# Kernel tuning notes

Measured on AMD Instinct MI355X. Metric: run time of the kernel, lower is better.

## Reference

```python
import jax, jax.numpy as jnp
import numpy as np

B, NIN, H1, H2, NOUT, COND, FC = 64, 512, 1024, 1024, 512, 64, 1


def _made_masks():
    rng = np.random.RandomState(0)
    d_in = np.arange(1, NIN + 1)
    d1 = rng.randint(1, NIN, size=H1)
    d2 = rng.randint(1, NIN, size=H2)
    d_out = np.arange(1, NOUT + 1)
    m0 = (d1[:, None] >= d_in[None, :]).astype(np.float32)   # (H1, NIN)
    m1 = (d2[:, None] >= d1[None, :]).astype(np.float32)     # (H2, H1)
    m2 = (d_out[:, None] > d2[None, :]).astype(np.float32)   # (NOUT, H2)
    return m0, m1, m2


def setup_inputs() -> dict:
    key = jax.random.key(0)
    ks = jax.random.split(key, 20)
    m0, m1, m2 = _made_masks()

    def lin(k, o, i):  # fan-in scaled weight
        return jax.random.normal(k, (o, i), jnp.float32) / np.float32(np.sqrt(i))

    def vec(k, n):
        return jax.random.normal(k, (n,), jnp.float32) * 0.01

    return {
        "x": jax.random.normal(ks[0], (B, NIN), jnp.float32),
        "u": jax.random.normal(ks[1], (B, COND), jnp.float32),
        "mask0": jnp.asarray(m0), "mask1": jnp.asarray(m1), "mask2": jnp.asarray(m2),
        "W0": lin(ks[2], H1, NIN), "W1": lin(ks[3], H2, H1), "W2": lin(ks[4], NOUT, H2),
        "a0_w": lin(ks[5], FC * NIN, COND), "a0_b": vec(ks[6], FC * NIN),
        "b0_w": lin(ks[7], FC * H1, COND), "b0_b": vec(ks[8], FC * H1),
        "a1_w": lin(ks[9], FC * H1, COND), "a1_b": vec(ks[10], FC * H1),
        "b1_w": lin(ks[11], FC * H2, COND), "b1_b": vec(ks[12], FC * H2),
        "a2_w": lin(ks[13], FC * H2, COND), "a2_b": vec(ks[14], FC * H2),
        "b2_w": lin(ks[15], FC * NOUT, COND), "b2_b": vec(ks[16], FC * NOUT),
    }


def _cml(x, u, W, m, aw, ab, bw, bb):
    # ConditionedMaskedLinear.forward
    Bb = x.shape[0]
    o, i = W.shape
    f1 = (u @ aw.T + ab).reshape(Bb, FC, i)      # (B, F, in)
    f2 = (u @ bw.T + bb).reshape(Bb, o, FC)      # (B, out, F)
    cond_mask = jax.nn.sigmoid(jnp.einsum('bfi,bof->boi', f1, f2)) * (m * W)
    return jnp.einsum('boi,bi->bo', cond_mask, x)


def reference(x, u, mask0, mask1, mask2, W0, W1, W2,
              a0_w, a0_b, b0_w, b0_b,
              a1_w, a1_b, b1_w, b1_b,
              a2_w, a2_b, b2_w, b2_b):
    # ConditionalStrNN.forward applies ONLY the ConditionedMaskedLinear layers
    # (activations/norms in net_list are skipped by the isinstance check).
    h = _cml(x, u, W0, mask0, a0_w, a0_b, b0_w, b0_b)
    h = _cml(h, u, W1, mask1, a1_w, a1_b, b1_w, b1_b)
    h = _cml(h, u, W2, mask2, a2_w, a2_b, b2_w, b2_b)
    return h
```

## Files before the change

### kernel.cpp

```cpp
#include <hip/hip_runtime.h>

#define BB    64
#define NIN   512
#define H1D   1024
#define H2D   1024
#define NOUTD 512
#define CONDD 64
#define L2E   1.4426950408889634f

__global__ __launch_bounds__(256) void prep_kernel(
    const float* __restrict__ x,  const float* __restrict__ u,
    const float* __restrict__ a0w, const float* __restrict__ a0b,
    const float* __restrict__ b0w, const float* __restrict__ b0b,
    const float* __restrict__ a1w, const float* __restrict__ a1b,
    const float* __restrict__ b1w, const float* __restrict__ b1b,
    const float* __restrict__ a2w, const float* __restrict__ a2b,
    const float* __restrict__ b2w, const float* __restrict__ b2b,
    const float* __restrict__ m0, const float* __restrict__ m1,
    const float* __restrict__ m2,
    float* __restrict__ AX0, float* __restrict__ AX1, float* __restrict__ AX2,
    float* __restrict__ C0t, float* __restrict__ C1t, float* __restrict__ C2t,
    int* __restrict__ len1, int* __restrict__ len2, int* __restrict__ len3,
    int* __restrict__ key2)
{
    __shared__ float lds[64 * 65];
    const int tid = threadIdx.x;
    const int bid = blockIdx.x;

    if (bid < 320) {
        for (int e = tid; e < BB * CONDD; e += 256)
            lds[(e & 63) * 65 + (e >> 6)] = u[e];
        __syncthreads();

        const int b   = tid & 63;
        const int wid = __builtin_amdgcn_readfirstlane(tid >> 6);
        const int r0  = bid * 16 + wid * 4;

        const float* w; const float* bias; float* o; int stride; float scale; int lr0;
        if      (r0 <  512) { w = a0w; bias = a0b; o = AX0; stride = 2; scale = L2E; lr0 = r0;        }
        else if (r0 < 1536) { w = b0w; bias = b0b; o = C0t; stride = 1; scale = 1.f; lr0 = r0 -  512; }
        else if (r0 < 2560) { w = a1w; bias = a1b; o = AX1; stride = 2; scale = L2E; lr0 = r0 - 1536; }
        else if (r0 < 3584) { w = b1w; bias = b1b; o = C1t; stride = 1; scale = 1.f; lr0 = r0 - 2560; }
        else if (r0 < 4608) { w = a2w; bias = a2b; o = AX2; stride = 2; scale = L2E; lr0 = r0 - 3584; }
        else                { w = b2w; bias = b2b; o = C2t; stride = 1; scale = 1.f; lr0 = r0 - 4608; }

        const float* __restrict__ w0 = w + (lr0 + 0) * CONDD;
        const float* __restrict__ w1 = w + (lr0 + 1) * CONDD;
        const float* __restrict__ w2 = w + (lr0 + 2) * CONDD;
        const float* __restrict__ w3 = w + (lr0 + 3) * CONDD;
        float acc0 = bias[lr0 + 0], acc1 = bias[lr0 + 1];
        float acc2 = bias[lr0 + 2], acc3 = bias[lr0 + 3];
        #pragma unroll
        for (int k = 0; k < CONDD; ++k) {
            const float uv = lds[k * 65 + b];
            acc0 = fmaf(w0[k], uv, acc0);
            acc1 = fmaf(w1[k], uv, acc1);
            acc2 = fmaf(w2[k], uv, acc2);
            acc3 = fmaf(w3[k], uv, acc3);
        }
        o[((lr0 + 0) * 64 + b) * stride] = acc0 * scale;
        o[((lr0 + 1) * 64 + b) * stride] = acc1 * scale;
        o[((lr0 + 2) * 64 + b) * stride] = acc2 * scale;
        o[((lr0 + 3) * 64 + b) * stride] = acc3 * scale;
    } else if (bid < 328) {
        const int i0 = (bid - 320) * 64;
        for (int e = tid; e < 64 * 64; e += 256) {
            int r = e >> 6, c = e & 63;
            lds[c * 65 + r] = x[r * NIN + i0 + c];
        }
        __syncthreads();
        for (int e = tid; e < 64 * 64; e += 256) {
            int r = e >> 6, c = e & 63;
            AX0[((i0 + r) * 64 + c) * 2 + 1] = lds[r * 65 + c];
        }
    } else if (bid < 392) {
        const int l = tid & 63, w = tid >> 6;
        const int rb = (bid - 328) * 16 + w * 4;
        for (int j = 0; j < 4; ++j) {
            const int r = rb + j;
            const float4* rp = (const float4*)(m0 + (size_t)r * 512);
            const float4 A = rp[l], B = rp[l + 64];
            float s = A.x + A.y + A.z + A.w + B.x + B.y + B.z + B.w;
            #pragma unroll
            for (int d = 32; d; d >>= 1) s += __shfl_down(s, d);
            if (l == 0) len1[r] = (int)(s + 0.5f);
        }
    } else if (bid < 456) {
        const int l = tid & 63, w = tid >> 6;
        const int rb = (bid - 392) * 16 + w * 4;
        for (int j = 0; j < 4; ++j) {
            const int r = rb + j;
            const float4* rp = (const float4*)(m1 + (size_t)r * 1024);
            const float4 A = rp[l], B = rp[l + 64], C = rp[l + 128], D = rp[l + 192];
            float s = A.x + A.y + A.z + A.w + B.x + B.y + B.z + B.w
                    + C.x + C.y + C.z + C.w + D.x + D.y + D.z + D.w;
            #pragma unroll
            for (int d = 32; d; d >>= 1) s += __shfl_down(s, d);
            if (l == 0) len2[r] = (int)(s + 0.5f);
        }
    } else if (bid < 488) {
        const int l = tid & 63, w = tid >> 6;
        const int rb = (bid - 456) * 16 + w * 4;
        for (int j = 0; j < 4; ++j) {
            const int r = rb + j;
            const float4* rp = (const float4*)(m2 + (size_t)r * 1024);
            const float4 A = rp[l], B = rp[l + 64], C = rp[l + 128], D = rp[l + 192];
            float s = A.x + A.y + A.z + A.w + B.x + B.y + B.z + B.w
                    + C.x + C.y + C.z + C.w + D.x + D.y + D.z + D.w;
            #pragma unroll
            for (int d = 32; d; d >>= 1) s += __shfl_down(s, d);
            if (l == 0) len3[r] = (int)(s + 0.5f);
        }
    } else {
        const int cb  = bid - 488;
        const int c   = cb * 64 + (tid & 63);
        const int seg = tid >> 6;
        float s = 0.f;
        for (int j = 0; j < 128; ++j)
            s += m2[(size_t)(seg * 128 + j) * 1024 + c];
        lds[seg * 64 + (tid & 63)] = s;
        __syncthreads();
        if (tid < 64) {
            const float t = lds[tid] + lds[64 + tid] + lds[128 + tid] + lds[192 + tid];
            key2[cb * 64 + tid] = 512 - (int)(t + 0.5f);
        }
    }
}

__global__ __launch_bounds__(1024) void sort_kernel(
    const int* __restrict__ len1, const int* __restrict__ key2,
    const int* __restrict__ len2,
    int* __restrict__ order1, int* __restrict__ len1s,
    int* __restrict__ order2, int* __restrict__ len2s)
{
    __shared__ int hist[1024];
    __shared__ int scan[1024];
    const int t = threadIdx.x;
    const int* key = blockIdx.x ? key2 : len1;
    const int k = key[t];
    hist[t] = 0;
    __syncthreads();
    atomicAdd(&hist[k], 1);
    __syncthreads();
    scan[t] = hist[t];
    __syncthreads();
    for (int s = 1; s < 1024; s <<= 1) {
        const int v = scan[t] + ((t >= s) ? scan[t - s] : 0);
        __syncthreads();
        scan[t] = v;
        __syncthreads();
    }
    const int excl = scan[t] - hist[t];
    __syncthreads();
    hist[t] = excl;
    __syncthreads();
    const int pos = atomicAdd(&hist[k], 1);
    if (blockIdx.x == 0) {
        order1[pos] = t;
        len1s[pos]  = k;
    } else {
        order2[pos] = t;
        len2s[pos]  = len2[t];
    }
}

template<int I, int O, bool PR, bool GI, bool FINAL>
__global__ __launch_bounds__(1024) void gated(
    const float2* __restrict__ AX, const float* __restrict__ Ct,
    const float* __restrict__ W,  const int* __restrict__ lenS,
    const int* __restrict__ ordRow, const int* __restrict__ ordIn,
    float* __restrict__ out)
{
    constexpr int NB = O / 2;
    const int bid = blockIdx.x;
    const int k   = (bid < NB / 2) ? bid : (NB + NB / 2 - 1 - bid);
    const int R0  = 2 * k;
    const int tid = threadIdx.x;
    const int b   = tid & 63;
    const int wid = __builtin_amdgcn_readfirstlane(tid >> 6);

    __shared__ float2 mw[I];
    __shared__ int    ord[GI ? I : 1];
    __shared__ float  red[16][2][64];

    const int len0 = lenS[R0], len1 = lenS[R0 + 1];
    const int r0 = PR ? ordRow[R0]     : R0;
    const int r1 = PR ? ordRow[R0 + 1] : (R0 + 1);
    const int Lb  = (len0 > len1) ? len0 : len1;
    const int T   = (Lb + 15) >> 4;
    const int T16 = T << 4;

    const float* __restrict__ w0p = W + (size_t)r0 * I;
    const float* __restrict__ w1p = W + (size_t)r1 * I;
    for (int p = tid; p < T16; p += 1024) {
        const int ix = GI ? ordIn[p] : p;
        if (GI) ord[p] = ix;
        float2 v;
        v.x = (p < len0) ? w0p[ix] : 0.f;
        v.y = (p < len1) ? w1p[ix] : 0.f;
        mw[p] = v;
    }
    const float cc0 = Ct[r0 * 64 + b];
    const float cc1 = Ct[r1 * 64 + b];
    __syncthreads();

    float a0 = 0.f, a1 = 0.f;
    #pragma unroll 4
    for (int t = 0; t < T; ++t) {
        const int p  = wid + (t << 4);
        const int ix = GI ? ord[p] : p;
        const float2 ax = AX[(size_t)ix * 64 + b];
        const float2 w  = mw[p];
        const float e0 = __builtin_amdgcn_exp2f(-(ax.x * cc0));
        const float s0 = __builtin_amdgcn_rcpf(1.f + e0);
        const float e1 = __builtin_amdgcn_exp2f(-(ax.x * cc1));
        const float s1 = __builtin_amdgcn_rcpf(1.f + e1);
        a0 = fmaf(s0, w.x * ax.y, a0);
        a1 = fmaf(s1, w.y * ax.y, a1);
    }

    red[wid][0][b] = a0;
    red[wid][1][b] = a1;
    __syncthreads();
    if (tid < 128) {
        const int oo = tid >> 6, bb = tid & 63;
        float v = 0.f;
        #pragma unroll
        for (int q = 0; q < 16; ++q) v += red[q][oo][bb];
        const int r = oo ? r1 : r0;
        if (FINAL) out[bb * NOUTD + r] = v;
        else       out[((size_t)r * 64 + bb) * 2 + 1] = v;
    }
}

extern "C" void kernel_launch(void* const* d_in, const int* in_sizes, int n_in,
                              void* d_out, int out_size, void* d_ws, size_t ws_size,
                              hipStream_t stream) {
    (void)in_sizes; (void)n_in; (void)out_size; (void)ws_size;
    const float* x   = (const float*)d_in[0];
    const float* u   = (const float*)d_in[1];
    const float* m0  = (const float*)d_in[2];
    const float* m1  = (const float*)d_in[3];
    const float* m2  = (const float*)d_in[4];
    const float* W0  = (const float*)d_in[5];
    const float* W1  = (const float*)d_in[6];
    const float* W2  = (const float*)d_in[7];
    const float* a0w = (const float*)d_in[8];  const float* a0b = (const float*)d_in[9];
    const float* b0w = (const float*)d_in[10]; const float* b0b = (const float*)d_in[11];
    const float* a1w = (const float*)d_in[12]; const float* a1b = (const float*)d_in[13];
    const float* b1w = (const float*)d_in[14]; const float* b1b = (const float*)d_in[15];
    const float* a2w = (const float*)d_in[16]; const float* a2b = (const float*)d_in[17];
    const float* b2w = (const float*)d_in[18]; const float* b2b = (const float*)d_in[19];

    float* ws  = (float*)d_ws;
    float* AX0 = ws;
    float* AX1 = ws + 65536;
    float* AX2 = ws + 196608;
    float* C0t = ws + 327680;
    float* C1t = ws + 393216;
    float* C2t = ws + 458752;
    int*   ib  = (int*)(ws + 491520);
    int* len1   = ib;
    int* len2   = ib + 1024;
    int* len3   = ib + 2048;
    int* key2   = ib + 2560;
    int* order1 = ib + 3584;
    int* len1s  = ib + 4608;
    int* order2 = ib + 5632;
    int* len2s  = ib + 6656;
    float* out = (float*)d_out;

    prep_kernel<<<504, 256, 0, stream>>>(x, u,
        a0w, a0b, b0w, b0b, a1w, a1b, b1w, b1b, a2w, a2b, b2w, b2b,
        m0, m1, m2,
        AX0, AX1, AX2, C0t, C1t, C2t,
        len1, len2, len3, key2);

    sort_kernel<<<2, 1024, 0, stream>>>(len1, key2, len2,
                                        order1, len1s, order2, len2s);

    gated<NIN, H1D, true,  false, false><<<H1D / 2, 1024, 0, stream>>>(
        (const float2*)AX0, C0t, W0, len1s, order1, nullptr, AX1);
    gated<H1D, H2D, true,  true,  false><<<H2D / 2, 1024, 0, stream>>>(
        (const float2*)AX1, C1t, W1, len2s, order2, order1, AX2);
    gated<H2D, NOUTD, false, true, true><<<NOUTD / 2, 1024, 0, stream>>>(
        (const float2*)AX2, C2t, W2, len3, nullptr, order2, out);
}
```

Before: 144.1 us.

## Store next-layer activations in sorted order to remove gathers and use contiguous per-wave chunks

Each middle layer now writes its (A, x) pairs indexed by sorted row position, pairing its output with the next layer's precomputed A term. The next layer can then read AX contiguously without the ordIn gather from LDS. Each wave handles a contiguous chunk of the reduction with float4 weight loads and more independent accumulators, and the final layer becomes a 512-thread, one-row-per-block kernel. Zeroed padding regions, written by an extra sort-kernel block, let the chunked loops read past the valid length safely. The cost is extra workspace and a more complex indexing scheme.

After: 140.7 us. 1.02x faster.

```diff
diff --git a/kernel.cpp b/kernel.cpp
--- a/kernel.cpp
+++ b/kernel.cpp
@@ -18,7 +18,7 @@
     const float* __restrict__ b2w, const float* __restrict__ b2b,
     const float* __restrict__ m0, const float* __restrict__ m1,
     const float* __restrict__ m2,
-    float* __restrict__ AX0, float* __restrict__ AX1, float* __restrict__ AX2,
+    float* __restrict__ AX0, float* __restrict__ A1x, float* __restrict__ A2x,
     float* __restrict__ C0t, float* __restrict__ C1t, float* __restrict__ C2t,
     int* __restrict__ len1, int* __restrict__ len2, int* __restrict__ len3,
     int* __restrict__ key2)
@@ -39,9 +39,9 @@
         const float* w; const float* bias; float* o; int stride; float scale; int lr0;
         if      (r0 <  512) { w = a0w; bias = a0b; o = AX0; stride = 2; scale = L2E; lr0 = r0;        }
         else if (r0 < 1536) { w = b0w; bias = b0b; o = C0t; stride = 1; scale = 1.f; lr0 = r0 -  512; }
-        else if (r0 < 2560) { w = a1w; bias = a1b; o = AX1; stride = 2; scale = L2E; lr0 = r0 - 1536; }
+        else if (r0 < 2560) { w = a1w; bias = a1b; o = A1x; stride = 1; scale = L2E; lr0 = r0 - 1536; }
         else if (r0 < 3584) { w = b1w; bias = b1b; o = C1t; stride = 1; scale = 1.f; lr0 = r0 - 2560; }
-        else if (r0 < 4608) { w = a2w; bias = a2b; o = AX2; stride = 2; scale = L2E; lr0 = r0 - 3584; }
+        else if (r0 < 4608) { w = a2w; bias = a2b; o = A2x; stride = 1; scale = L2E; lr0 = r0 - 3584; }
         else                { w = b2w; bias = b2b; o = C2t; stride = 1; scale = 1.f; lr0 = r0 - 4608; }
 
         const float* __restrict__ w0 = w + (lr0 + 0) * CONDD;
@@ -131,8 +131,21 @@
     const int* __restrict__ len1, const int* __restrict__ key2,
     const int* __restrict__ len2,
     int* __restrict__ order1, int* __restrict__ len1s,
-    int* __restrict__ order2, int* __restrict__ len2s)
+    int* __restrict__ order2, int* __restrict__ len2s,
+    float4* __restrict__ pad0, float4* __restrict__ pad1,
+    float4* __restrict__ pad2)
 {
+    if (blockIdx.x == 2) {
+        const float4 z = {0.f, 0.f, 0.f, 0.f};
+        const int t = threadIdx.x;
+        #pragma unroll
+        for (int j = 0; j < 2; ++j) {
+            pad0[j * 1024 + t] = z;
+            pad1[j * 1024 + t] = z;
+            pad2[j * 1024 + t] = z;
+        }
+        return;
+    }
     __shared__ int hist[1024];
     __shared__ int scan[1024];
     const int t = threadIdx.x;
@@ -164,63 +177,64 @@
     }
 }
 
-template<int I, int O, bool PR, bool GI, bool FINAL>
-__global__ __launch_bounds__(1024) void gated(
+template<int I, bool GI>
+__global__ __launch_bounds__(1024) void gated_mid(
     const float2* __restrict__ AX, const float* __restrict__ Ct,
-    const float* __restrict__ W,  const int* __restrict__ lenS,
-    const int* __restrict__ ordRow, const int* __restrict__ ordIn,
-    float* __restrict__ out)
+    const float* __restrict__ W,  const float* __restrict__ Anext,
+    const int* __restrict__ lenS, const int* __restrict__ ordRow,
+    const int* __restrict__ ordIn, float2* __restrict__ outAX)
 {
-    constexpr int NB = O / 2;
     const int bid = blockIdx.x;
-    const int k   = (bid < NB / 2) ? bid : (NB + NB / 2 - 1 - bid);
+    const int k   = (bid < 256) ? bid : (767 - bid);
     const int R0  = 2 * k;
     const int tid = threadIdx.x;
     const int b   = tid & 63;
     const int wid = __builtin_amdgcn_readfirstlane(tid >> 6);
 
-    __shared__ float2 mw[I];
-    __shared__ int    ord[GI ? I : 1];
+    __shared__ float2 mw2[I + 64];
     __shared__ float  red[16][2][64];
 
     const int len0 = lenS[R0], len1 = lenS[R0 + 1];
-    const int r0 = PR ? ordRow[R0]     : R0;
-    const int r1 = PR ? ordRow[R0 + 1] : (R0 + 1);
-    const int Lb  = (len0 > len1) ? len0 : len1;
-    const int T   = (Lb + 15) >> 4;
-    const int T16 = T << 4;
+    const int r0 = ordRow[R0], r1 = ordRow[R0 + 1];
+    const int Lmax = (len0 > len1) ? len0 : len1;
+    const int Q = ((((Lmax + 1) >> 1) + 15) >> 4);
+    const int S = Q << 5;
 
     const float* __restrict__ w0p = W + (size_t)r0 * I;
     const float* __restrict__ w1p = W + (size_t)r1 * I;
-    for (int p = tid; p < T16; p += 1024) {
-        const int ix = GI ? ordIn[p] : p;
-        if (GI) ord[p] = ix;
+    for (int p = tid; p < S; p += 1024) {
+        const int ix = GI ? ((p < Lmax) ? ordIn[p] : 0) : p;
         float2 v;
         v.x = (p < len0) ? w0p[ix] : 0.f;
         v.y = (p < len1) ? w1p[ix] : 0.f;
-        mw[p] = v;
+        mw2[p] = v;
     }
     const float cc0 = Ct[r0 * 64 + b];
     const float cc1 = Ct[r1 * 64 + b];
     __syncthreads();
 
-    float a0 = 0.f, a1 = 0.f;
+    const int base = (wid * Q) << 1;
+    const float2* __restrict__ axp = AX + (size_t)base * 64 + b;
+    const float2* __restrict__ mwp = mw2 + base;
+
+    float a00 = 0.f, a01 = 0.f, a10 = 0.f, a11 = 0.f;
     #pragma unroll 4
-    for (int t = 0; t < T; ++t) {
-        const int p  = wid + (t << 4);
-        const int ix = GI ? ord[p] : p;
-        const float2 ax = AX[(size_t)ix * 64 + b];
-        const float2 w  = mw[p];
-        const float e0 = __builtin_amdgcn_exp2f(-(ax.x * cc0));
-        const float s0 = __builtin_amdgcn_rcpf(1.f + e0);
-        const float e1 = __builtin_amdgcn_exp2f(-(ax.x * cc1));
-        const float s1 = __builtin_amdgcn_rcpf(1.f + e1);
-        a0 = fmaf(s0, w.x * ax.y, a0);
-        a1 = fmaf(s1, w.y * ax.y, a1);
-    }
-
-    red[wid][0][b] = a0;
-    red[wid][1][b] = a1;
+    for (int t = 0; t < Q; ++t) {
+        const float4 m4  = *(const float4*)(mwp + 2 * t);
+        const float2 axa = axp[(size_t)(2 * t) * 64];
+        const float2 axb = axp[(size_t)(2 * t + 1) * 64];
+        const float e0 = __builtin_amdgcn_exp2f(-(axa.x * cc0));
+        const float e1 = __builtin_amdgcn_exp2f(-(axa.x * cc1));
+        const float e2 = __builtin_amdgcn_exp2f(-(axb.x * cc0));
+        const float e3 = __builtin_amdgcn_exp2f(-(axb.x * cc1));
+        a00 = fmaf(__builtin_amdgcn_rcpf(1.f + e0), m4.x * axa.y, a00);
+        a01 = fmaf(__builtin_amdgcn_rcpf(1.f + e1), m4.y * axa.y, a01);
+        a10 = fmaf(__builtin_amdgcn_rcpf(1.f + e2), m4.z * axb.y, a10);
+        a11 = fmaf(__builtin_amdgcn_rcpf(1.f + e3), m4.w * axb.y, a11);
+    }
+
+    red[wid][0][b] = a00 + a10;
+    red[wid][1][b] = a01 + a11;
     __syncthreads();
     if (tid < 128) {
         const int oo = tid >> 6, bb = tid & 63;
@@ -228,8 +242,66 @@
         #pragma unroll
         for (int q = 0; q < 16; ++q) v += red[q][oo][bb];
         const int r = oo ? r1 : r0;
-        if (FINAL) out[bb * NOUTD + r] = v;
-        else       out[((size_t)r * 64 + bb) * 2 + 1] = v;
+        float2 o2;
+        o2.x = Anext[r * 64 + bb];
+        o2.y = v;
+        outAX[(size_t)(R0 + oo) * 64 + bb] = o2;
+    }
+}
+
+__global__ __launch_bounds__(512) void gated_fin(
+    const float2* __restrict__ AX, const float* __restrict__ Ct,
+    const float* __restrict__ W,  const int* __restrict__ len3,
+    const int* __restrict__ ordIn, float* __restrict__ out)
+{
+    const int bid = blockIdx.x;
+    const int r   = (bid < 256) ? bid : (767 - bid);
+    const int tid = threadIdx.x;
+    const int b   = tid & 63;
+    const int wid = __builtin_amdgcn_readfirstlane(tid >> 6);
+
+    __shared__ float mw1[H2D + 64];
+    __shared__ float red[8][64];
+
+    const int len = len3[r];
+    const int Q   = (((len + 3) >> 2) + 7) >> 3;
+    const int S   = Q << 5;
+
+    const float* __restrict__ wp = W + (size_t)r * H2D;
+    for (int p = tid; p < S; p += 512)
+        mw1[p] = (p < len) ? wp[ordIn[p]] : 0.f;
+    const float cc = Ct[r * 64 + b];
+    __syncthreads();
+
+    const int base = (wid * Q) << 2;
+    const float2* __restrict__ axp = AX + (size_t)base * 64 + b;
+    const float*  __restrict__ mwp = mw1 + base;
+
+    float a0 = 0.f, a1 = 0.f, a2 = 0.f, a3 = 0.f;
+    #pragma unroll 4
+    for (int t = 0; t < Q; ++t) {
+        const float4 mm  = *(const float4*)(mwp + 4 * t);
+        const float2 x0 = axp[(size_t)(4 * t + 0) * 64];
+        const float2 x1 = axp[(size_t)(4 * t + 1) * 64];
+        const float2 x2 = axp[(size_t)(4 * t + 2) * 64];
+        const float2 x3 = axp[(size_t)(4 * t + 3) * 64];
+        const float e0 = __builtin_amdgcn_exp2f(-(x0.x * cc));
+        const float e1 = __builtin_amdgcn_exp2f(-(x1.x * cc));
+        const float e2 = __builtin_amdgcn_exp2f(-(x2.x * cc));
+        const float e3 = __builtin_amdgcn_exp2f(-(x3.x * cc));
+        a0 = fmaf(__builtin_amdgcn_rcpf(1.f + e0), mm.x * x0.y, a0);
+        a1 = fmaf(__builtin_amdgcn_rcpf(1.f + e1), mm.y * x1.y, a1);
+        a2 = fmaf(__builtin_amdgcn_rcpf(1.f + e2), mm.z * x2.y, a2);
+        a3 = fmaf(__builtin_amdgcn_rcpf(1.f + e3), mm.w * x3.y, a3);
+    }
+
+    red[wid][b] = (a0 + a1) + (a2 + a3);
+    __syncthreads();
+    if (tid < 64) {
+        float v = 0.f;
+        #pragma unroll
+        for (int q = 0; q < 8; ++q) v += red[q][tid];
+        out[tid * NOUTD + r] = v;
     }
 }
 
@@ -252,14 +324,16 @@
     const float* a2w = (const float*)d_in[16]; const float* a2b = (const float*)d_in[17];
     const float* b2w = (const float*)d_in[18]; const float* b2b = (const float*)d_in[19];
 
-    float* ws  = (float*)d_ws;
-    float* AX0 = ws;
-    float* AX1 = ws + 65536;
-    float* AX2 = ws + 196608;
-    float* C0t = ws + 327680;
-    float* C1t = ws + 393216;
-    float* C2t = ws + 458752;
-    int*   ib  = (int*)(ws + 491520);
+    float* ws   = (float*)d_ws;
+    float* AX0  = ws;
+    float* AX1s = ws + 73728;
+    float* AX2s = ws + 212992;
+    float* A1x  = ws + 352256;
+    float* A2x  = ws + 417792;
+    float* C0t  = ws + 483328;
+    float* C1t  = ws + 548864;
+    float* C2t  = ws + 614400;
+    int*   ib   = (int*)(ws + 647168);
     int* len1   = ib;
     int* len2   = ib + 1024;
     int* len3   = ib + 2048;
@@ -268,21 +342,28 @@
     int* len1s  = ib + 4608;
     int* order2 = ib + 5632;
     int* len2s  = ib + 6656;
-    float* out = (float*)d_out;
+    float* out  = (float*)d_out;
+
+    float4* pad0 = (float4*)(AX0  + 512 * 64 * 2);
+    float4* pad1 = (float4*)(AX1s + 1024 * 64 * 2);
+    float4* pad2 = (float4*)(AX2s + 1024 * 64 * 2);
 
     prep_kernel<<<504, 256, 0, stream>>>(x, u,
         a0w, a0b, b0w, b0b, a1w, a1b, b1w, b1b, a2w, a2b, b2w, b2b,
         m0, m1, m2,
-        AX0, AX1, AX2, C0t, C1t, C2t,
+        AX0, A1x, A2x, C0t, C1t, C2t,
         len1, len2, len3, key2);
 
-    sort_kernel<<<2, 1024, 0, stream>>>(len1, key2, len2,
-                                        order1, len1s, order2, len2s);
-
-    gated<NIN, H1D, true,  false, false><<<H1D / 2, 1024, 0, stream>>>(
-        (const float2*)AX0, C0t, W0, len1s, order1, nullptr, AX1);
-    gated<H1D, H2D, true,  true,  false><<<H2D / 2, 1024, 0, stream>>>(
-        (const float2*)AX1, C1t, W1, len2s, order2, order1, AX2);
-    gated<H2D, NOUTD, false, true, true><<<NOUTD / 2, 1024, 0, stream>>>(
-        (const float2*)AX2, C2t, W2, len3, nullptr, order2, out);
-}
+    sort_kernel<<<3, 1024, 0, stream>>>(len1, key2, len2,
+                                        order1, len1s, order2, len2s,
+                                        pad0, pad1, pad2);
+
+    gated_mid<NIN, false><<<512, 1024, 0, stream>>>(
+        (const float2*)AX0, C0t, W0, A1x, len1s, order1, nullptr,
+        (float2*)AX1s);
+    gated_mid<H1D, true><<<512, 1024, 0, stream>>>(
+        (const float2*)AX1s, C1t, W1, A2x, len2s, order2, order1,
+        (float2*)AX2s);
+    gated_fin<<<512, 512, 0, stream>>>(
+        (const float2*)AX2s, C2t, W2, len3, order2, out);
+}
```
